# Kernel tuning notes

Hardware: AMD Instinct MI355X
Metric: run time of the kernel (lower is better)

Reference implementation:

```python
import jax, jax.numpy as jnp
import numpy as np

E = 2      # expansion
G = 8      # groups
K = 128    # num_clusters
N = 1024   # feature_size (dim)
D = E * N // G  # per-group cluster dim = 256
EPS = 1e-12


def _l2norm(v, axis):
    return v / jnp.maximum(jnp.linalg.norm(v, axis=axis, keepdims=True), EPS)


def setup_inputs() -> dict:
    key = jax.random.key(0)
    ks = jax.random.split(key, 8)
    x = jax.random.normal(ks[0], (64, N, 8, 8), dtype=jnp.float32)
    W_inp = jax.random.normal(ks[1], (E * N, N), dtype=jnp.float32) * 0.02
    b_inp = jax.random.uniform(ks[2], (E * N,), dtype=jnp.float32)
    W_g = jax.random.normal(ks[3], (G, E * N), dtype=jnp.float32) * 0.02
    b_g = jax.random.uniform(ks[4], (G,), dtype=jnp.float32)
    W_gk = jax.random.normal(ks[5], (G * K, E * N), dtype=jnp.float32) * 0.02
    b_gk = jax.random.uniform(ks[6], (G * K,), dtype=jnp.float32)
    centroids = jax.random.normal(ks[7], (K, D), dtype=jnp.float32) * 0.1
    return {"x": x, "W_inp": W_inp, "b_inp": b_inp, "W_g": W_g, "b_g": b_g,
            "W_gk": W_gk, "b_gk": b_gk, "centroids": centroids}


def reference(x, W_inp, b_inp, W_g, b_g, W_gk, b_gk, centroids):
    b8, c, h, w = x.shape
    bs = b8 // 8
    # [bs*8, C, H, W] -> [bs, M=8*H*W, N=C]
    x = x.reshape(bs, 8, c, h, w).transpose(0, 2, 1, 3, 4).reshape(bs, c, 8 * h * w)
    x = jnp.transpose(x, (0, 2, 1))            # [bs, M, N]
    M = x.shape[1]
    x = _l2norm(x, axis=2)                     # normalize_input
    x = x @ W_inp.T + b_inp                    # [bs, M, E*N]
    alpha_g = jax.nn.sigmoid(x @ W_g.T + b_g)  # [bs, M, G]
    # NOTE: original uses Softmax(dim=1) -> softmax over token dim M
    alpha_gk = jax.nn.softmax(x @ W_gk.T + b_gk, axis=1)   # [bs, M, G*K]
    alpha_gk = alpha_gk.reshape(bs, M, G, K)
    xr = x.reshape(bs, M, G, D)
    w_full = alpha_g[..., None] * alpha_gk     # [bs, M, G, K]
    # vlad[b,k,d] = sum_{m,g} w*(x - c) = einsum(w,x) - (sum w) * c
    vlad = jnp.einsum('bmgk,bmgd->bkd', w_full, xr) \
        - jnp.sum(w_full, axis=(1, 2))[..., None] * centroids  # [bs, K, D]
    vlad = _l2norm(vlad, axis=-1).reshape(bs, K * D)
    return _l2norm(vlad, axis=1)
```

## Files before the change

### kernel.cpp

```cpp
#include <hip/hip_runtime.h>
#include <hip/hip_bf16.h>
#include <math.h>

#define EPSN 1e-12f
typedef unsigned short ushort_t;

typedef float f32x4 __attribute__((ext_vector_type(4)));
typedef short s16x8 __attribute__((ext_vector_type(8)));
typedef unsigned short u16x8 __attribute__((ext_vector_type(8)));
typedef unsigned short u16x4 __attribute__((ext_vector_type(4)));

__device__ __forceinline__ void gload_lds16(const void* g, void* l) {
  __builtin_amdgcn_global_load_lds((const __attribute__((address_space(1))) void*)g,
                                   (__attribute__((address_space(3))) void*)l, 16, 0, 0);
}

__global__ void k0_ssq(const float* __restrict__ x, float* __restrict__ ssq8) {
  int b8 = blockIdx.x >> 3;
  int cc = blockIdx.x & 7;
  int t = threadIdx.x;
  int s4 = (t & 15) * 4;
  int cg = t >> 4;
  const float* xp = x + (size_t)b8 * 65536 + (size_t)cc * 128 * 64;
  float4 a = {0.f, 0.f, 0.f, 0.f};
#pragma unroll
  for (int j = 0; j < 8; ++j) {
    int c = cg + j * 16;
    float4 v = *(const float4*)(xp + (size_t)c * 64 + s4);
    a.x = fmaf(v.x, v.x, a.x);
    a.y = fmaf(v.y, v.y, a.y);
    a.z = fmaf(v.z, v.z, a.z);
    a.w = fmaf(v.w, v.w, a.w);
  }
  __shared__ float red[16][68];
  *(float4*)&red[cg][s4] = a;
  __syncthreads();
  if (t < 64) {
    float s = 0.f;
#pragma unroll
    for (int g = 0; g < 16; ++g) s += red[g][t];
    ssq8[cc * 4096 + b8 * 64 + t] = s;
  }
}

__global__ void k1_transpose(const float* __restrict__ x, const float* __restrict__ ssq8,
                             __hip_bfloat16* __restrict__ xnb) {
  int ct = blockIdx.x;
  int b8 = blockIdx.y;
  int t = threadIdx.x;
  __shared__ float tile[64][65];
  __shared__ float ivs[64];
  if (t < 64) {
    float s = 0.f;
#pragma unroll
    for (int cc = 0; cc < 8; ++cc) s += ssq8[cc * 4096 + b8 * 64 + t];
    ivs[t] = rsqrtf(fmaxf(s, 1e-24f));
  }
  int s = t & 63, cq = t >> 6;
  const float* xp = x + (size_t)b8 * 65536 + (size_t)ct * 64 * 64;
#pragma unroll
  for (int r = 0; r < 16; ++r) {
    int cl = cq * 16 + r;
    tile[cl][s] = xp[cl * 64 + s];
  }
  __syncthreads();
  int cl = t & 63, sq = t >> 6;
#pragma unroll
  for (int r = 0; r < 16; ++r) {
    int smm = sq * 16 + r;
    int tm = b8 * 64 + smm;
    xnb[(size_t)tm * 1024 + ct * 64 + cl] = __float2bfloat16(tile[cl][smm] * ivs[smm]);
  }
}

__global__ void kpack2(const float* __restrict__ Wi, const float* __restrict__ Wgk,
                       const float* __restrict__ W_g, const float* __restrict__ b_inp,
                       const float* __restrict__ b_g, __hip_bfloat16* __restrict__ oWi,
                       __hip_bfloat16* __restrict__ oWx, ushort_t* __restrict__ oWibT,
                       float* __restrict__ bWg) {
  int bid = blockIdx.x;
  int t = threadIdx.x;
  if (bid < 2048) {
    int i = (bid * 256 + t) * 4;
    float4 v = *(const float4*)(Wi + i);
    oWi[i + 0] = __float2bfloat16(v.x);
    oWi[i + 1] = __float2bfloat16(v.y);
    oWi[i + 2] = __float2bfloat16(v.z);
    oWi[i + 3] = __float2bfloat16(v.w);
  } else if (bid < 4096) {
    int i = ((bid - 2048) * 256 + t) * 4;
    float4 v = *(const float4*)(Wgk + i);
    oWx[i + 0] = __float2bfloat16(v.x);
    oWx[i + 1] = __float2bfloat16(v.y);
    oWx[i + 2] = __float2bfloat16(v.z);
    oWx[i + 3] = __float2bfloat16(v.w);
  } else if (bid < 4112) {
    int i = (bid - 4096) * 1024 + t * 4;
    float4 v = *(const float4*)(W_g + i);
    __hip_bfloat16* o = oWx + 1024 * 2048 + i;
    o[0] = __float2bfloat16(v.x);
    o[1] = __float2bfloat16(v.y);
    o[2] = __float2bfloat16(v.z);
    o[3] = __float2bfloat16(v.w);
  } else if (bid < 4352) {
    int i = (bid - 4112) * 1024 + t * 4;
    ushort_t* o = (ushort_t*)(oWx + 1032 * 2048) + i;
    *(u16x4*)o = (u16x4){0, 0, 0, 0};
  } else if (bid < 4360) {
    int j = bid - 4352;
    const float* row = W_g + (size_t)j * 2048;
    float s = 0.f;
    for (int c = t; c < 2048; c += 256) s = fmaf(b_inp[c], row[c], s);
    __shared__ float red[256];
    red[t] = s;
    __syncthreads();
    for (int o = 128; o > 0; o >>= 1) {
      if (t < o) red[t] += red[t + o];
      __syncthreads();
    }
    if (t == 0) bWg[j] = red[0] + b_g[j];
  } else {
    int tt = bid - 4360;
    int cp0 = (tt >> 4) * 64;
    int c0 = (tt & 15) * 64;
    __shared__ ushort_t tile[64][72];
    int r = t >> 2, cs = (t & 3) * 16;
    const float* src = Wi + (size_t)(cp0 + r) * 1024 + c0 + cs;
#pragma unroll
    for (int j = 0; j < 16; j += 4) {
      float4 v = *(const float4*)(src + j);
      __hip_bfloat16 h0 = __float2bfloat16(v.x), h1 = __float2bfloat16(v.y);
      __hip_bfloat16 h2 = __float2bfloat16(v.z), h3 = __float2bfloat16(v.w);
      tile[r][cs + j + 0] = *(ushort_t*)&h0;
      tile[r][cs + j + 1] = *(ushort_t*)&h1;
      tile[r][cs + j + 2] = *(ushort_t*)&h2;
      tile[r][cs + j + 3] = *(ushort_t*)&h3;
    }
    __syncthreads();
    int c = t >> 2, ms = (t & 3) * 16;
    u16x8 o0, o1;
#pragma unroll
    for (int j = 0; j < 8; ++j) o0[j] = tile[ms + j][c];
#pragma unroll
    for (int j = 0; j < 8; ++j) o1[j] = tile[ms + 8 + j][c];
    ushort_t* dst = oWibT + (size_t)(c0 + c) * 2048 + cp0 + ms;
    *(u16x8*)dst = o0;
    *(u16x8*)(dst + 8) = o1;
  }
}

__launch_bounds__(512, 4)
__global__ void gemm_nt_bf16(const ushort_t* __restrict__ A, const ushort_t* __restrict__ B,
                             ushort_t* __restrict__ C, int K, int N) {
  __shared__ alignas(16) ushort_t SH[32768];
  const int tid = threadIdx.x;
  const int m0 = blockIdx.y * 128, n0 = blockIdx.x * 128;
  const int w = tid >> 6, l = tid & 63;
  const int wr = w >> 2, wc = w & 3;
  const int srow = w * 8 + (l >> 3);
  const int ksw = ((l & 7) ^ (l >> 3)) * 8;
  const ushort_t* Ag0 = A + (size_t)(m0 + srow) * K + ksw;
  const ushort_t* Ag1 = A + (size_t)(m0 + 64 + srow) * K + ksw;
  const ushort_t* Bg0 = B + (size_t)(n0 + srow) * K + ksw;
  const ushort_t* Bg1 = B + (size_t)(n0 + 64 + srow) * K + ksw;
  const int l0 = w * 512;
  const int l1 = 4096 + w * 512;

  f32x4 acc[4][2];
#pragma unroll
  for (int i = 0; i < 4; ++i)
#pragma unroll
    for (int j = 0; j < 2; ++j) acc[i][j] = (f32x4){0.f, 0.f, 0.f, 0.f};

  const int sw = l & 7, qq = l >> 4;

#define ASH(buf) (SH + (buf)*8192)
#define BSH(buf) (SH + 16384 + (buf)*8192)
#define STAGE(buf, k0)                               \
  {                                                  \
    gload_lds16(Ag0 + (k0), ASH(buf) + l0);          \
    gload_lds16(Ag1 + (k0), ASH(buf) + l1);          \
    gload_lds16(Bg0 + (k0), BSH(buf) + l0);          \
    gload_lds16(Bg1 + (k0), BSH(buf) + l1);          \
  }

#define COMPUTE(buf)                                                                     \
  {                                                                                      \
    s16x8 af[4][2], bf[2][2];                                                            \
    _Pragma("unroll") for (int kk = 0; kk < 2; ++kk) {                                   \
      int slot = (((kk << 2) + qq) ^ sw) * 8;                                            \
      _Pragma("unroll") for (int mi = 0; mi < 4; ++mi)                                   \
          af[mi][kk] = *(const s16x8*)&ASH(buf)[(wr * 64 + mi * 16 + (l & 15)) * 64 +    \
                                               slot];                                   \
      _Pragma("unroll") for (int ni = 0; ni < 2; ++ni)                                   \
          bf[ni][kk] = *(const s16x8*)&BSH(buf)[(wc * 32 + ni * 16 + (l & 15)) * 64 +    \
                                               slot];                                   \
    }                                                                                    \
    _Pragma("unroll") for (int kk = 0; kk < 2; ++kk)                                     \
        _Pragma("unroll") for (int mi = 0; mi < 4; ++mi)                                 \
            _Pragma("unroll") for (int ni = 0; ni < 2; ++ni)                             \
                acc[mi][ni] = __builtin_amdgcn_mfma_f32_16x16x32_bf16(af[mi][kk],        \
                                                                     bf[ni][kk],        \
                                                                     acc[mi][ni], 0, 0, 0); \
  }

  const int nt = K >> 6;
  STAGE(0, 0);
  int buf = 0;
  for (int t = 0; t < nt - 1; ++t) {
    STAGE(buf ^ 1, (t + 1) << 6);
    asm volatile("s_waitcnt vmcnt(4)" ::: "memory");
    __builtin_amdgcn_s_barrier();
    asm volatile("" ::: "memory");
    COMPUTE(buf);
    asm volatile("" ::: "memory");
    __builtin_amdgcn_s_barrier();
    buf ^= 1;
  }
  asm volatile("s_waitcnt vmcnt(0)" ::: "memory");
  __builtin_amdgcn_s_barrier();
  asm volatile("" ::: "memory");
  COMPUTE(buf);
#undef STAGE
#undef COMPUTE
#undef ASH
#undef BSH

#pragma unroll
  for (int mi = 0; mi < 4; ++mi) {
    int row = m0 + wr * 64 + mi * 16 + (l >> 4) * 4;
#pragma unroll
    for (int ni = 0; ni < 2; ++ni) {
      int col = n0 + wc * 32 + ni * 16 + (l & 15);
#pragma unroll
      for (int r = 0; r < 4; ++r) {
        __hip_bfloat16 hb = __float2bfloat16(acc[mi][ni][r]);
        C[(size_t)(row + r) * N + col] = *(ushort_t*)&hb;
      }
    }
  }
}

__launch_bounds__(256)
__global__ void k5_softmax(const ushort_t* __restrict__ logitsTb, const float* __restrict__ bWg,
                           float* __restrict__ colsumW, ushort_t* __restrict__ wbT) {
  int wv = (blockIdx.x << 2) + (threadIdx.x >> 6);
  int q = wv >> 3, b = wv & 7;
  int l = threadIdx.x & 63;
  int g = q >> 7;
  size_t base = (size_t)q * 4096 + b * 512 + l * 8;
  u16x8 v8 = *(const u16x8*)(logitsTb + base);
  float vs[8];
#pragma unroll
  for (int i = 0; i < 8; ++i) vs[i] = __uint_as_float(((unsigned)v8[i]) << 16);
  float M = vs[0];
#pragma unroll
  for (int i = 1; i < 8; ++i) M = fmaxf(M, vs[i]);
#pragma unroll
  for (int m = 1; m < 64; m <<= 1) M = fmaxf(M, __shfl_xor(M, m, 64));
  float e[8], S = 0.f;
#pragma unroll
  for (int i = 0; i < 8; ++i) {
    e[i] = expf(vs[i] - M);
    S += e[i];
  }
#pragma unroll
  for (int m = 1; m < 64; m <<= 1) S += __shfl_xor(S, m, 64);
  float R = 1.0f / S;
  u16x8 g8 = *(const u16x8*)(logitsTb + (size_t)(1024 + g) * 4096 + b * 512 + l * 8);
  float bg = bWg[g];
  float wv8[8], wsum = 0.f;
#pragma unroll
  for (int i = 0; i < 8; ++i) {
    float gl = __uint_as_float(((unsigned)g8[i]) << 16);
    float ag = 1.0f / (1.0f + expf(-(gl + bg)));
    wv8[i] = e[i] * R * ag;
    wsum += wv8[i];
  }
#pragma unroll
  for (int m = 1; m < 64; m <<= 1) wsum += __shfl_xor(wsum, m, 64);
  if (l == 0) colsumW[b * 1024 + q] = wsum;
  u16x8 o;
#pragma unroll
  for (int i = 0; i < 8; ++i) {
    __hip_bfloat16 hb = __float2bfloat16(wv8[i]);
    o[i] = *(ushort_t*)&hb;
  }
  *(u16x8*)(wbT + base) = o;
}

__launch_bounds__(256)
__global__ void k6_vlad_mfma(const ushort_t* __restrict__ wbT, const ushort_t* __restrict__ YcT,
                             float* __restrict__ vpart) {
  int kt = blockIdx.x >> 2, dt = blockIdx.x & 3;
  int ms = blockIdx.y, b = blockIdx.z;
  __shared__ alignas(16) ushort_t Ash[2][4096];
  __shared__ alignas(16) ushort_t Bsh[2][4096];
  const int tid = threadIdx.x;
  const int w = tid >> 6, l = tid & 63;
  const int wr = w >> 1, wc = w & 1;
  const int crow = l >> 3;
  const int ksw = ((l & 7) ^ crow) * 8;

  const ushort_t* Ap[2];
  const ushort_t* Bp[2];
  int loff[2];
#pragma unroll
  for (int c = 0; c < 2; ++c) {
    int chunk = w * 2 + c;
    Ap[c] = wbT + (size_t)(kt * 64 + chunk * 8 + crow) * 4096 + b * 512 + ms * 64 + ksw;
    Bp[c] = YcT + (size_t)(dt * 64 + chunk * 8 + crow) * 4096 + b * 512 + ms * 64 + ksw;
    loff[c] = chunk * 512;
  }

  f32x4 acc[2][2];
#pragma unroll
  for (int i = 0; i < 2; ++i)
#pragma unroll
    for (int j = 0; j < 2; ++j) acc[i][j] = (f32x4){0.f, 0.f, 0.f, 0.f};

  const int sw = l & 7, qq = l >> 4;

#define STAGE6(buf, g)                                                       \
  {                                                                          \
    size_t offA = (size_t)(g)*524288;                                        \
    size_t offB = (size_t)(g)*1048576;                                       \
    gload_lds16(Ap[0] + offA, &Ash[buf][loff[0]]);                           \
    gload_lds16(Ap[1] + offA, &Ash[buf][loff[1]]);                           \
    gload_lds16(Bp[0] + offB, &Bsh[buf][loff[0]]);                           \
    gload_lds16(Bp[1] + offB, &Bsh[buf][loff[1]]);                           \
  }

#define COMPUTE6(buf)                                                                    \
  {                                                                                      \
    s16x8 af[2][2], bf[2][2];                                                            \
    _Pragma("unroll") for (int kk = 0; kk < 2; ++kk) {                                   \
      int slot = (((kk << 2) + qq) ^ sw) * 8;                                            \
      _Pragma("unroll") for (int mi = 0; mi < 2; ++mi) {                                 \
        af[mi][kk] = *(const s16x8*)&Ash[buf][(wr * 32 + mi * 16 + (l & 15)) * 64 +      \
                                             slot];                                     \
        bf[mi][kk] = *(const s16x8*)&Bsh[buf][(wc * 32 + mi * 16 + (l & 15)) * 64 +      \
                                             slot];                                     \
      }                                                                                  \
    }                                                                                    \
    _Pragma("unroll") for (int kk = 0; kk < 2; ++kk)                                     \
        _Pragma("unroll") for (int mi = 0; mi < 2; ++mi)                                 \
            _Pragma("unroll") for (int ni = 0; ni < 2; ++ni)                             \
                acc[mi][ni] = __builtin_amdgcn_mfma_f32_16x16x32_bf16(af[mi][kk],        \
                                                                     bf[ni][kk],        \
                                                                     acc[mi][ni], 0, 0, 0); \
  }

  STAGE6(0, 0);
  int buf = 0;
  for (int s = 0; s < 7; ++s) {
    STAGE6(buf ^ 1, s + 1);
    asm volatile("s_waitcnt vmcnt(4)" ::: "memory");
    __builtin_amdgcn_s_barrier();
    asm volatile("" ::: "memory");
    COMPUTE6(buf);
    asm volatile("" ::: "memory");
    __builtin_amdgcn_s_barrier();
    buf ^= 1;
  }
  asm volatile("s_waitcnt vmcnt(0)" ::: "memory");
  __builtin_amdgcn_s_barrier();
  asm volatile("" ::: "memory");
  COMPUTE6(buf);
#undef STAGE6
#undef COMPUTE6

#pragma unroll
  for (int mi = 0; mi < 2; ++mi) {
    int row = kt * 64 + wr * 32 + mi * 16 + (l >> 4) * 4;
#pragma unroll
    for (int ni = 0; ni < 2; ++ni) {
      int col = dt * 64 + wc * 32 + ni * 16 + (l & 15);
#pragma unroll
      for (int r = 0; r < 4; ++r)
        vpart[((size_t)(ms * 8 + b) * 128 + row + r) * 256 + col] = acc[mi][ni][r];
    }
  }
}

__global__ void k7_intranorm(const float* __restrict__ vpart, const float* __restrict__ colsumW,
                             const float* __restrict__ b_inp, const float* __restrict__ cent,
                             float* __restrict__ out, float* __restrict__ ss1) {
  int k = blockIdx.x;
  int b = blockIdx.y;
  int d = threadIdx.x;
  float S = 0.f, bp = 0.f;
#pragma unroll
  for (int g = 0; g < 8; ++g) {
    float cw = colsumW[b * 1024 + g * 128 + k];
    S += cw;
    bp = fmaf(b_inp[g * 256 + d], cw, bp);
  }
  size_t off = ((size_t)b * 128 + k) * 256 + d;
  float v = bp - S * cent[(size_t)k * 256 + d];
#pragma unroll
  for (int i = 0; i < 8; ++i) v += vpart[off + (size_t)i * 262144];
  float ss = v * v;
#pragma unroll
  for (int m = 1; m < 64; m <<= 1) ss += __shfl_xor(ss, m, 64);
  __shared__ float red[4];
  int lane = d & 63, wv = d >> 6;
  if (lane == 0) red[wv] = ss;
  __syncthreads();
  float tot = red[0] + red[1] + red[2] + red[3];
  float rinv = 1.0f / fmaxf(sqrtf(tot), EPSN);
  out[off] = v * rinv;
  if (d == 0) ss1[b * 128 + k] = tot * rinv * rinv;
}

__global__ void k8_finalnorm(const float* __restrict__ ss1, float* __restrict__ out) {
  int b = blockIdx.x;
  int t = threadIdx.x;
  __shared__ float red[256];
  red[t] = (t < 128) ? ss1[b * 128 + t] : 0.f;
  __syncthreads();
  for (int o = 128; o > 0; o >>= 1) {
    if (t < o) red[t] += red[t + o];
    __syncthreads();
  }
  float rinv = 1.0f / fmaxf(sqrtf(red[0]), EPSN);
  float* op = out + (size_t)b * 32768;
  for (int i = t; i < 32768; i += 256) op[i] *= rinv;
}

extern "C" void kernel_launch(void* const* d_in, const int* in_sizes, int n_in,
                              void* d_out, int out_size, void* d_ws, size_t ws_size,
                              hipStream_t stream) {
  const float* x     = (const float*)d_in[0];
  const float* W_inp = (const float*)d_in[1];
  const float* b_inp = (const float*)d_in[2];
  const float* W_g   = (const float*)d_in[3];
  const float* b_g   = (const float*)d_in[4];
  const float* W_gk  = (const float*)d_in[5];
  const float* cent  = (const float*)d_in[7];
  float* out = (float*)d_out;
  float* ws = (float*)d_ws;

  float* ssq8    = ws + 0;
  float* colsumW = ws + 32768;
  float* ss1     = ws + 40960;
  float* bWg     = ws + 41984;
  __hip_bfloat16* xnb = (__hip_bfloat16*)(ws + 42048);
  ushort_t* wbT  = (ushort_t*)xnb;
  __hip_bfloat16* Wib  = (__hip_bfloat16*)(ws + 2139200);
  ushort_t* WibT = (ushort_t*)(ws + 3187776);
  float* vpart   = ws + 2139200;
  __hip_bfloat16* Wgkx   = (__hip_bfloat16*)(ws + 4236352);
  __hip_bfloat16* Wcombx = (__hip_bfloat16*)(ws + 5416000);
  ushort_t* YcT  = (ushort_t*)(ws + 6005824);
  ushort_t* logitsTb = (ushort_t*)(ws + 10200128);

  k0_ssq<<<512, 256, 0, stream>>>(x, ssq8);
  k1_transpose<<<dim3(16, 64), 256, 0, stream>>>(x, ssq8, xnb);
  kpack2<<<4872, 256, 0, stream>>>(W_inp, W_gk, W_g, b_inp, b_g, Wib, Wgkx, WibT, bWg);
  gemm_nt_bf16<<<dim3(8, 9), 512, 0, stream>>>((const ushort_t*)Wgkx, WibT,
                                               (ushort_t*)Wcombx, 2048, 1024);
  gemm_nt_bf16<<<dim3(32, 16), 512, 0, stream>>>((const ushort_t*)Wib, (const ushort_t*)xnb,
                                                 YcT, 1024, 4096);
  gemm_nt_bf16<<<dim3(32, 9), 512, 0, stream>>>((const ushort_t*)Wcombx, (const ushort_t*)xnb,
                                                logitsTb, 1024, 4096);
  k5_softmax<<<2048, 256, 0, stream>>>(logitsTb, bWg, colsumW, wbT);
  k6_vlad_mfma<<<dim3(8, 8, 8), 256, 0, stream>>>(wbT, YcT, vpart);
  k7_intranorm<<<dim3(128, 8), 256, 0, stream>>>(vpart, colsumW, b_inp, cent, out, ss1);
  k8_finalnorm<<<8, 256, 0, stream>>>(ss1, out);
}
```

Measured before the change: 128.1 us.

## Split-K the weight-combine GEMM and merge the two activation GEMMs into one launch

The small Wgk·Wib GEMM (72 blocks) becomes a 4-way split-K kernel with 288 blocks writing fp32 partials. A new pack kernel sums the partials, converts them to bf16 and writes them directly below the W_inp block in a stacked A matrix. The two separate GEMMs against xnb then run as one 800-block launch producing YcT and logits contiguously. This targets low occupancy in the first GEMM and removes one launch and its tail effect, at the cost of an extra fp32 partial round trip and an additional kernel.

```diff
diff --git a/kernel.cpp b/kernel.cpp
--- a/kernel.cpp
+++ b/kernel.cpp
@@ -150,19 +150,22 @@
 }
 
 __launch_bounds__(512, 4)
-__global__ void gemm_nt_bf16(const ushort_t* __restrict__ A, const ushort_t* __restrict__ B,
-                             ushort_t* __restrict__ C, int K, int N) {
+__global__ void gemm0_splitk(const ushort_t* __restrict__ A, const ushort_t* __restrict__ B,
+                             float* __restrict__ Cf) {
+  const int Kstride = 2048, N = 1024;
   __shared__ alignas(16) ushort_t SH[32768];
   const int tid = threadIdx.x;
   const int m0 = blockIdx.y * 128, n0 = blockIdx.x * 128;
+  const int s = blockIdx.z;
+  const int koff = s * 512;
   const int w = tid >> 6, l = tid & 63;
   const int wr = w >> 2, wc = w & 3;
   const int srow = w * 8 + (l >> 3);
   const int ksw = ((l & 7) ^ (l >> 3)) * 8;
-  const ushort_t* Ag0 = A + (size_t)(m0 + srow) * K + ksw;
-  const ushort_t* Ag1 = A + (size_t)(m0 + 64 + srow) * K + ksw;
-  const ushort_t* Bg0 = B + (size_t)(n0 + srow) * K + ksw;
-  const ushort_t* Bg1 = B + (size_t)(n0 + 64 + srow) * K + ksw;
+  const ushort_t* Ag0 = A + (size_t)(m0 + srow) * Kstride + ksw + koff;
+  const ushort_t* Ag1 = A + (size_t)(m0 + 64 + srow) * Kstride + ksw + koff;
+  const ushort_t* Bg0 = B + (size_t)(n0 + srow) * Kstride + ksw + koff;
+  const ushort_t* Bg1 = B + (size_t)(n0 + 64 + srow) * Kstride + ksw + koff;
   const int l0 = w * 512;
   const int l1 = 4096 + w * 512;
 
@@ -183,7 +186,6 @@
     gload_lds16(Bg0 + (k0), BSH(buf) + l0);          \
     gload_lds16(Bg1 + (k0), BSH(buf) + l1);          \
   }
-
 #define COMPUTE(buf)                                                                     \
   {                                                                                      \
     s16x8 af[4][2], bf[2][2];                                                            \
@@ -204,6 +206,111 @@
                                                                      acc[mi][ni], 0, 0, 0); \
   }
 
+  STAGE(0, 0);
+  int buf = 0;
+  for (int t = 0; t < 7; ++t) {
+    STAGE(buf ^ 1, (t + 1) << 6);
+    asm volatile("s_waitcnt vmcnt(4)" ::: "memory");
+    __builtin_amdgcn_s_barrier();
+    asm volatile("" ::: "memory");
+    COMPUTE(buf);
+    asm volatile("" ::: "memory");
+    __builtin_amdgcn_s_barrier();
+    buf ^= 1;
+  }
+  asm volatile("s_waitcnt vmcnt(0)" ::: "memory");
+  __builtin_amdgcn_s_barrier();
+  asm volatile("" ::: "memory");
+  COMPUTE(buf);
+#undef STAGE
+#undef COMPUTE
+#undef ASH
+#undef BSH
+
+  float* Co = Cf + (size_t)s * 1152 * 1024;
+#pragma unroll
+  for (int mi = 0; mi < 4; ++mi) {
+    int row = m0 + wr * 64 + mi * 16 + (l >> 4) * 4;
+#pragma unroll
+    for (int ni = 0; ni < 2; ++ni) {
+      int col = n0 + wc * 32 + ni * 16 + (l & 15);
+#pragma unroll
+      for (int r = 0; r < 4; ++r)
+        Co[(size_t)(row + r) * N + col] = acc[mi][ni][r];
+    }
+  }
+}
+
+__global__ void kpackC(const float* __restrict__ Wc4, ushort_t* __restrict__ dst) {
+  int i = (blockIdx.x * 256 + threadIdx.x) * 4;
+  float4 a = *(const float4*)(Wc4 + i);
+  float4 b = *(const float4*)(Wc4 + 1179648 + i);
+  float4 c = *(const float4*)(Wc4 + 2359296 + i);
+  float4 d = *(const float4*)(Wc4 + 3538944 + i);
+  float4 sv = {a.x + b.x + c.x + d.x, a.y + b.y + c.y + d.y,
+               a.z + b.z + c.z + d.z, a.w + b.w + c.w + d.w};
+  u16x4 o;
+  __hip_bfloat16 h0 = __float2bfloat16(sv.x), h1 = __float2bfloat16(sv.y);
+  __hip_bfloat16 h2 = __float2bfloat16(sv.z), h3 = __float2bfloat16(sv.w);
+  o[0] = *(ushort_t*)&h0; o[1] = *(ushort_t*)&h1;
+  o[2] = *(ushort_t*)&h2; o[3] = *(ushort_t*)&h3;
+  *(u16x4*)(dst + i) = o;
+}
+
+__launch_bounds__(512, 4)
+__global__ void gemm_nt_bf16(const ushort_t* __restrict__ A, const ushort_t* __restrict__ B,
+                             ushort_t* __restrict__ C, int K, int N) {
+  __shared__ alignas(16) ushort_t SH[32768];
+  const int tid = threadIdx.x;
+  const int m0 = blockIdx.y * 128, n0 = blockIdx.x * 128;
+  const int w = tid >> 6, l = tid & 63;
+  const int wr = w >> 2, wc = w & 3;
+  const int srow = w * 8 + (l >> 3);
+  const int ksw = ((l & 7) ^ (l >> 3)) * 8;
+  const ushort_t* Ag0 = A + (size_t)(m0 + srow) * K + ksw;
+  const ushort_t* Ag1 = A + (size_t)(m0 + 64 + srow) * K + ksw;
+  const ushort_t* Bg0 = B + (size_t)(n0 + srow) * K + ksw;
+  const ushort_t* Bg1 = B + (size_t)(n0 + 64 + srow) * K + ksw;
+  const int l0 = w * 512;
+  const int l1 = 4096 + w * 512;
+
+  f32x4 acc[4][2];
+#pragma unroll
+  for (int i = 0; i < 4; ++i)
+#pragma unroll
+    for (int j = 0; j < 2; ++j) acc[i][j] = (f32x4){0.f, 0.f, 0.f, 0.f};
+
+  const int sw = l & 7, qq = l >> 4;
+
+#define ASH(buf) (SH + (buf)*8192)
+#define BSH(buf) (SH + 16384 + (buf)*8192)
+#define STAGE(buf, k0)                               \
+  {                                                  \
+    gload_lds16(Ag0 + (k0), ASH(buf) + l0);          \
+    gload_lds16(Ag1 + (k0), ASH(buf) + l1);          \
+    gload_lds16(Bg0 + (k0), BSH(buf) + l0);          \
+    gload_lds16(Bg1 + (k0), BSH(buf) + l1);          \
+  }
+#define COMPUTE(buf)                                                                     \
+  {                                                                                      \
+    s16x8 af[4][2], bf[2][2];                                                            \
+    _Pragma("unroll") for (int kk = 0; kk < 2; ++kk) {                                   \
+      int slot = (((kk << 2) + qq) ^ sw) * 8;                                            \
+      _Pragma("unroll") for (int mi = 0; mi < 4; ++mi)                                   \
+          af[mi][kk] = *(const s16x8*)&ASH(buf)[(wr * 64 + mi * 16 + (l & 15)) * 64 +    \
+                                               slot];                                   \
+      _Pragma("unroll") for (int ni = 0; ni < 2; ++ni)                                   \
+          bf[ni][kk] = *(const s16x8*)&BSH(buf)[(wc * 32 + ni * 16 + (l & 15)) * 64 +    \
+                                               slot];                                   \
+    }                                                                                    \
+    _Pragma("unroll") for (int kk = 0; kk < 2; ++kk)                                     \
+        _Pragma("unroll") for (int mi = 0; mi < 4; ++mi)                                 \
+            _Pragma("unroll") for (int ni = 0; ni < 2; ++ni)                             \
+                acc[mi][ni] = __builtin_amdgcn_mfma_f32_16x16x32_bf16(af[mi][kk],        \
+                                                                     bf[ni][kk],        \
+                                                                     acc[mi][ni], 0, 0, 0); \
+  }
+
   const int nt = K >> 6;
   STAGE(0, 0);
   int buf = 0;
@@ -330,7 +437,6 @@
     gload_lds16(Bp[0] + offB, &Bsh[buf][loff[0]]);                           \
     gload_lds16(Bp[1] + offB, &Bsh[buf][loff[1]]);                           \
   }
-
 #define COMPUTE6(buf)                                                                    \
   {                                                                                      \
     s16x8 af[2][2], bf[2][2];                                                            \
@@ -445,25 +551,24 @@
   float* colsumW = ws + 32768;
   float* ss1     = ws + 40960;
   float* bWg     = ws + 41984;
-  __hip_bfloat16* xnb = (__hip_bfloat16*)(ws + 42048);
-  ushort_t* wbT  = (ushort_t*)xnb;
-  __hip_bfloat16* Wib  = (__hip_bfloat16*)(ws + 2139200);
-  ushort_t* WibT = (ushort_t*)(ws + 3187776);
-  float* vpart   = ws + 2139200;
-  __hip_bfloat16* Wgkx   = (__hip_bfloat16*)(ws + 4236352);
-  __hip_bfloat16* Wcombx = (__hip_bfloat16*)(ws + 5416000);
-  ushort_t* YcT  = (ushort_t*)(ws + 6005824);
-  ushort_t* logitsTb = (ushort_t*)(ws + 10200128);
+  ushort_t* xnb  = (ushort_t*)(ws + 42048);
+  ushort_t* wbT  = xnb;
+  ushort_t* stackedA = (ushort_t*)(ws + 2139200);
+  ushort_t* WibT = (ushort_t*)(ws + 3777600);
+  ushort_t* Wgkx = (ushort_t*)(ws + 4826176);
+  float* vpart   = ws + 3777600;
+  float* Wc4     = ws + 6005824;
+  ushort_t* Cstacked = (ushort_t*)(ws + 6005824);
+  ushort_t* YcT      = Cstacked;
+  ushort_t* logitsTb = Cstacked + (size_t)2048 * 4096;
 
   k0_ssq<<<512, 256, 0, stream>>>(x, ssq8);
-  k1_transpose<<<dim3(16, 64), 256, 0, stream>>>(x, ssq8, xnb);
-  kpack2<<<4872, 256, 0, stream>>>(W_inp, W_gk, W_g, b_inp, b_g, Wib, Wgkx, WibT, bWg);
-  gemm_nt_bf16<<<dim3(8, 9), 512, 0, stream>>>((const ushort_t*)Wgkx, WibT,
-                                               (ushort_t*)Wcombx, 2048, 1024);
-  gemm_nt_bf16<<<dim3(32, 16), 512, 0, stream>>>((const ushort_t*)Wib, (const ushort_t*)xnb,
-                                                 YcT, 1024, 4096);
-  gemm_nt_bf16<<<dim3(32, 9), 512, 0, stream>>>((const ushort_t*)Wcombx, (const ushort_t*)xnb,
-                                                logitsTb, 1024, 4096);
+  k1_transpose<<<dim3(16, 64), 256, 0, stream>>>(x, ssq8, (__hip_bfloat16*)xnb);
+  kpack2<<<4872, 256, 0, stream>>>(W_inp, W_gk, W_g, b_inp, b_g,
+                                   (__hip_bfloat16*)stackedA, (__hip_bfloat16*)Wgkx, WibT, bWg);
+  gemm0_splitk<<<dim3(8, 9, 4), 512, 0, stream>>>(Wgkx, WibT, Wc4);
+  kpackC<<<1152, 256, 0, stream>>>(Wc4, stackedA + (size_t)2048 * 1024);
+  gemm_nt_bf16<<<dim3(32, 25), 512, 0, stream>>>(stackedA, xnb, Cstacked, 1024, 4096);
   k5_softmax<<<2048, 256, 0, stream>>>(logitsTb, bWg, colsumW, wbT);
   k6_vlad_mfma<<<dim3(8, 8, 8), 256, 0, stream>>>(wbT, YcT, vpart);
   k7_intranorm<<<dim3(128, 8), 256, 0, stream>>>(vpart, colsumW, b_inp, cent, out, ss1);
```

Measured after the change: 123.1 us. -3.8%, faster.
